# Performance work log

Measured on AMD Instinct MI355X. Metric: run time of the kernel, lower is better.

Reference implementation:

```python
import jax, jax.numpy as jnp
import numpy as np

B, C, N, D, E = 2048, 3, 1568, 16, 8  # batch, classes, input caps, out dim, in dim
T_ROUTING = 3


def squash(t, axis=-1):
    sq_norm = jnp.sum(t * t, axis=axis, keepdims=True)
    return (sq_norm / (1.0 + sq_norm)) * t / jnp.sqrt(sq_norm)


def setup_inputs() -> dict:
    key = jax.random.key(0)
    k1, k2 = jax.random.split(key)
    x = jax.random.normal(k1, (B, N, E), dtype=jnp.float32)
    W = 0.001 * jax.random.normal(k2, (1, C, N, D, E), dtype=jnp.float32)
    return {"x": x, "W": W}


def reference(x, W):
    # u_hat = W @ x[:, None, :, :, None]  -> (B, C, N, D) (trailing 1-dim dropped)
    u = jnp.einsum('ocnde,bne->bcnd', W, x)
    b = jnp.zeros((B, C, N), dtype=u.dtype)  # routing logits
    v = None
    for _ in range(T_ROUTING):
        c = jax.nn.softmax(b, axis=1)               # coupling coeffs over classes
        s = jnp.einsum('bcnd,bcn->bcd', u, c)       # weighted sum over input caps
        v = squash(s)                               # (B, C, D)
        b = b + jnp.einsum('bcd,bcnd->bcn', v, u)   # agreement update
    return v
```

## Files before the change

kernel.cpp:

```cpp
#include <hip/hip_runtime.h>
#include <hip/hip_fp16.h>

#define BB 2048
#define NN 1568
#define CD 48

__device__ __forceinline__ unsigned packh2(float a, float b) {
    __half2 h = __floats2half2_rn(a, b);
    unsigned r; __builtin_memcpy(&r, &h, 4); return r;
}
__device__ __forceinline__ float2 uph2(unsigned v) {
    __half2 h; __builtin_memcpy(&h, &v, 4); return __half22float2(h);
}

__global__ __launch_bounds__(256, 3)
void k1_u(const float* __restrict__ x, const float* __restrict__ W,
          __half* __restrict__ u)
{
    __shared__ float wlds[16 * 384];
    const int t  = threadIdx.x;
    const int bl = t & 31;
    const int h  = (t >> 5) & 1;
    const int ns = t >> 6;
    const int bg = blockIdx.x & 63;
    const int g  = blockIdx.x >> 6;
    const int b  = bg * 32 + bl;
    const int n0 = g * 16;

    float xr[32];
#pragma unroll
    for (int i = 0; i < 4; ++i) {
        const float* xp = x + ((size_t)b * NN + n0 + ns * 4 + i) * 8;
        const float4 a = __ldg((const float4*)xp);
        const float4 c = __ldg((const float4*)(xp + 4));
        xr[i*8+0]=a.x; xr[i*8+1]=a.y; xr[i*8+2]=a.z; xr[i*8+3]=a.w;
        xr[i*8+4]=c.x; xr[i*8+5]=c.y; xr[i*8+6]=c.z; xr[i*8+7]=c.w;
    }

#pragma unroll
    for (int k = 0; k < 6; ++k) {
        const int q = t + k * 256;
        const int c = q >> 9;
        const int j = (q >> 5) & 15;
        const int f = q & 31;
        const float4 v = *(const float4*)(W + (((size_t)(c * NN + n0 + j)) << 7) + (f << 2));
        *(float4*)(wlds + j * 384 + c * 128 + (f << 2)) = v;
    }
    __syncthreads();

#pragma unroll
    for (int i = 0; i < 4; ++i) {
        const int nr = ns * 4 + i;
        const int n  = n0 + nr;
        const float x0 = xr[i*8+0], x1 = xr[i*8+1], x2 = xr[i*8+2], x3 = xr[i*8+3];
        const float x4 = xr[i*8+4], x5 = xr[i*8+5], x6 = xr[i*8+6], x7 = xr[i*8+7];
        __half* dst = u + ((size_t)b * NN + n) * CD + h * 8;

#pragma unroll
        for (int c = 0; c < 3; ++c) {
            const float* wc = wlds + nr * 384 + c * 128 + h * 64;
            uint4 pk;
#pragma unroll
            for (int pp = 0; pp < 4; ++pp) {
                const float4 w0 = *(const float4*)(wc + 16 * pp);
                const float4 w1 = *(const float4*)(wc + 16 * pp + 4);
                const float4 w2 = *(const float4*)(wc + 16 * pp + 8);
                const float4 w3 = *(const float4*)(wc + 16 * pp + 12);
                const float a0 = w0.x*x0 + w0.y*x1 + w0.z*x2 + w0.w*x3
                               + w1.x*x4 + w1.y*x5 + w1.z*x6 + w1.w*x7;
                const float a1 = w2.x*x0 + w2.y*x1 + w2.z*x2 + w2.w*x3
                               + w3.x*x4 + w3.y*x5 + w3.z*x6 + w3.w*x7;
                const unsigned pv = packh2(a0, a1);
                if (pp == 0) pk.x = pv; else if (pp == 1) pk.y = pv;
                else if (pp == 2) pk.z = pv; else pk.w = pv;
            }
            *(uint4*)(dst + c * 16) = pk;
        }
    }
}

__global__ __launch_bounds__(256, 3)
void k2_route(const __half* __restrict__ u, float* __restrict__ out)
{
    __shared__ float red[4][CD];
    __shared__ float vsh[CD];

    const int t = threadIdx.x;
    const int w = t >> 6;
    const int b = blockIdx.x;
    const __half* ub = u + (size_t)b * NN * CD;

    float acc[CD];

#pragma unroll
    for (int i = 0; i < CD; ++i) acc[i] = 0.f;
    for (int n = t; n < NN; n += 256) {
        const uint4* p = (const uint4*)(ub + (size_t)n * CD);
        const uint4 r0 = p[0], r1 = p[1], r2 = p[2], r3 = p[3], r4 = p[4], r5 = p[5];
        const unsigned rr[24] = { r0.x,r0.y,r0.z,r0.w, r1.x,r1.y,r1.z,r1.w,
                                  r2.x,r2.y,r2.z,r2.w, r3.x,r3.y,r3.z,r3.w,
                                  r4.x,r4.y,r4.z,r4.w, r5.x,r5.y,r5.z,r5.w };
#pragma unroll
        for (int j = 0; j < 24; ++j) {
            const float2 f = uph2(rr[j]);
            acc[2*j] += f.x; acc[2*j+1] += f.y;
        }
    }
#pragma unroll
    for (int i = 0; i < CD; ++i) {
        float v = acc[i];
        v += __shfl_xor(v, 1); v += __shfl_xor(v, 2); v += __shfl_xor(v, 4);
        v += __shfl_xor(v, 8); v += __shfl_xor(v, 16); v += __shfl_xor(v, 32);
        acc[i] = v;
    }
    if ((t & 63) == 0) { for (int i = 0; i < CD; ++i) red[w][i] = acc[i]; }
    __syncthreads();
    if (t < CD) {
        float s = (red[0][t] + red[1][t] + red[2][t] + red[3][t]) * (1.0f / 3.0f);
        float q = s * s;
        q += __shfl_xor(q, 1); q += __shfl_xor(q, 2); q += __shfl_xor(q, 4); q += __shfl_xor(q, 8);
        vsh[t] = s * sqrtf(q) / (1.f + q);
    }
    __syncthreads();

#pragma unroll 1
    for (int pass = 1; pass <= 2; ++pass) {
        float wv[CD];
#pragma unroll
        for (int i = 0; i < CD; ++i) wv[i] = vsh[i];
#pragma unroll
        for (int i = 0; i < CD; ++i) acc[i] = 0.f;

        for (int n = t; n < NN; n += 256) {
            const uint4* p = (const uint4*)(ub + (size_t)n * CD);
            const uint4 r0 = p[0], r1 = p[1], r2 = p[2], r3 = p[3], r4 = p[4], r5 = p[5];
            const unsigned rr[24] = { r0.x,r0.y,r0.z,r0.w, r1.x,r1.y,r1.z,r1.w,
                                      r2.x,r2.y,r2.z,r2.w, r3.x,r3.y,r3.z,r3.w,
                                      r4.x,r4.y,r4.z,r4.w, r5.x,r5.y,r5.z,r5.w };
            float l0 = 0.f, l1 = 0.f, l2 = 0.f;
#pragma unroll
            for (int j = 0; j < 8; ++j) {
                const float2 f0 = uph2(rr[j]);
                const float2 f1 = uph2(rr[8 + j]);
                const float2 f2 = uph2(rr[16 + j]);
                l0 += wv[2*j]      * f0.x + wv[2*j+1]      * f0.y;
                l1 += wv[16+2*j]   * f1.x + wv[16+2*j+1]   * f1.y;
                l2 += wv[32+2*j]   * f2.x + wv[32+2*j+1]   * f2.y;
            }
            const float e0 = __expf(l0), e1 = __expf(l1), e2 = __expf(l2);
            const float inv = 1.f / (e0 + e1 + e2);
            const float c0 = e0 * inv, c1 = e1 * inv, c2 = e2 * inv;
#pragma unroll
            for (int j = 0; j < 8; ++j) {
                const float2 f0 = uph2(rr[j]);
                const float2 f1 = uph2(rr[8 + j]);
                const float2 f2 = uph2(rr[16 + j]);
                acc[2*j]      += c0 * f0.x;  acc[2*j+1]      += c0 * f0.y;
                acc[16+2*j]   += c1 * f1.x;  acc[16+2*j+1]   += c1 * f1.y;
                acc[32+2*j]   += c2 * f2.x;  acc[32+2*j+1]   += c2 * f2.y;
            }
        }
#pragma unroll
        for (int i = 0; i < CD; ++i) {
            float v = acc[i];
            v += __shfl_xor(v, 1); v += __shfl_xor(v, 2); v += __shfl_xor(v, 4);
            v += __shfl_xor(v, 8); v += __shfl_xor(v, 16); v += __shfl_xor(v, 32);
            acc[i] = v;
        }
        if ((t & 63) == 0) { for (int i = 0; i < CD; ++i) red[w][i] = acc[i]; }
        __syncthreads();
        if (t < CD) {
            const float s = red[0][t] + red[1][t] + red[2][t] + red[3][t];
            float q = s * s;
            q += __shfl_xor(q, 1); q += __shfl_xor(q, 2); q += __shfl_xor(q, 4); q += __shfl_xor(q, 8);
            const float v = s * sqrtf(q) / (1.f + q);
            if (pass == 1) vsh[t] = wv[t] + v;
            else           out[b * CD + t] = v;
        }
        __syncthreads();
    }
}

extern "C" void kernel_launch(void* const* d_in, const int* in_sizes, int n_in,
                              void* d_out, int out_size, void* d_ws, size_t ws_size,
                              hipStream_t stream) {
    (void)in_sizes; (void)n_in; (void)out_size;
    const float* x = (const float*)d_in[0];
    const float* W = (const float*)d_in[1];
    const size_t u_bytes = (size_t)BB * NN * CD * sizeof(__half);
    if (ws_size < u_bytes) return;
    __half* u = (__half*)d_ws;

    hipLaunchKernelGGL(k1_u,     dim3(98 * 64), dim3(256), 0, stream, x, W, u);
    hipLaunchKernelGGL(k2_route, dim3(BB),      dim3(256), 0, stream, u, (float*)d_out);
}
```

Baseline: 435.4 us.

## Fuse u_hat computation into routing kernel with per-batch LDS-resident u

Removes the global fp16 u_hat buffer (about 300 MB written and then read three times). A small pre-kernel converts W to fp16 in a coalesced layout. Each batch block then computes u_hat into LDS (about 157 KB) and runs all routing passes from LDS. The cost is one block per CU with 512 threads, W being re-read from L2 by every batch block, and fp16 rounding of W, which adds error.

```diff
diff --git a/kernel.cpp b/kernel.cpp
--- a/kernel.cpp
+++ b/kernel.cpp
@@ -4,6 +4,8 @@
 #define BB 2048
 #define NN 1568
 #define CD 48
+#define TPB 512
+#define WSLOTS 98304
 
 __device__ __forceinline__ unsigned packh2(float a, float b) {
     __half2 h = __floats2half2_rn(a, b);
@@ -13,110 +15,110 @@
     __half2 h; __builtin_memcpy(&h, &v, 4); return __half22float2(h);
 }
 
-__global__ __launch_bounds__(256, 3)
-void k1_u(const float* __restrict__ x, const float* __restrict__ W,
-          __half* __restrict__ u)
+__global__ __launch_bounds__(256)
+void wcast(const float* __restrict__ W, uint4* __restrict__ Wh)
 {
-    __shared__ float wlds[16 * 384];
-    const int t  = threadIdx.x;
-    const int bl = t & 31;
-    const int h  = (t >> 5) & 1;
-    const int ns = t >> 6;
-    const int bg = blockIdx.x & 63;
-    const int g  = blockIdx.x >> 6;
-    const int b  = bg * 32 + bl;
-    const int n0 = g * 16;
-
-    float xr[32];
+    const int id = blockIdx.x * 256 + threadIdx.x;
+    const int ts = id & 511;
+    const int r  = id >> 9;
+    const int dq = r & 3;
+    const int ci = r >> 2;
+    const int i  = ci & 3;
+    const int c  = ci >> 2;
+    const int n  = i * 512 + ts;
+    uint4* dst = Wh + (size_t)ci * 8192 + dq * 4 * 512 + ts;
+    if (n < NN) {
+        const float* src = W + ((size_t)(c * NN + n)) * 128 + dq * 32;
 #pragma unroll
-    for (int i = 0; i < 4; ++i) {
-        const float* xp = x + ((size_t)b * NN + n0 + ns * 4 + i) * 8;
-        const float4 a = __ldg((const float4*)xp);
-        const float4 c = __ldg((const float4*)(xp + 4));
-        xr[i*8+0]=a.x; xr[i*8+1]=a.y; xr[i*8+2]=a.z; xr[i*8+3]=a.w;
-        xr[i*8+4]=c.x; xr[i*8+5]=c.y; xr[i*8+6]=c.z; xr[i*8+7]=c.w;
-    }
-
+        for (int dd = 0; dd < 4; ++dd) {
+            const float4 f0 = *(const float4*)(src + dd * 8);
+            const float4 f1 = *(const float4*)(src + dd * 8 + 4);
+            uint4 q;
+            q.x = packh2(f0.x, f0.y); q.y = packh2(f0.z, f0.w);
+            q.z = packh2(f1.x, f1.y); q.w = packh2(f1.z, f1.w);
+            dst[dd * 512] = q;
+        }
+    } else {
+        const uint4 z = make_uint4(0u, 0u, 0u, 0u);
 #pragma unroll
-    for (int k = 0; k < 6; ++k) {
-        const int q = t + k * 256;
-        const int c = q >> 9;
-        const int j = (q >> 5) & 15;
-        const int f = q & 31;
-        const float4 v = *(const float4*)(W + (((size_t)(c * NN + n0 + j)) << 7) + (f << 2));
-        *(float4*)(wlds + j * 384 + c * 128 + (f << 2)) = v;
-    }
-    __syncthreads();
-
-#pragma unroll
-    for (int i = 0; i < 4; ++i) {
-        const int nr = ns * 4 + i;
-        const int n  = n0 + nr;
-        const float x0 = xr[i*8+0], x1 = xr[i*8+1], x2 = xr[i*8+2], x3 = xr[i*8+3];
-        const float x4 = xr[i*8+4], x5 = xr[i*8+5], x6 = xr[i*8+6], x7 = xr[i*8+7];
-        __half* dst = u + ((size_t)b * NN + n) * CD + h * 8;
-
-#pragma unroll
-        for (int c = 0; c < 3; ++c) {
-            const float* wc = wlds + nr * 384 + c * 128 + h * 64;
-            uint4 pk;
-#pragma unroll
-            for (int pp = 0; pp < 4; ++pp) {
-                const float4 w0 = *(const float4*)(wc + 16 * pp);
-                const float4 w1 = *(const float4*)(wc + 16 * pp + 4);
-                const float4 w2 = *(const float4*)(wc + 16 * pp + 8);
-                const float4 w3 = *(const float4*)(wc + 16 * pp + 12);
-                const float a0 = w0.x*x0 + w0.y*x1 + w0.z*x2 + w0.w*x3
-                               + w1.x*x4 + w1.y*x5 + w1.z*x6 + w1.w*x7;
-                const float a1 = w2.x*x0 + w2.y*x1 + w2.z*x2 + w2.w*x3
-                               + w3.x*x4 + w3.y*x5 + w3.z*x6 + w3.w*x7;
-                const unsigned pv = packh2(a0, a1);
-                if (pp == 0) pk.x = pv; else if (pp == 1) pk.y = pv;
-                else if (pp == 2) pk.z = pv; else pk.w = pv;
-            }
-            *(uint4*)(dst + c * 16) = pk;
-        }
+        for (int dd = 0; dd < 4; ++dd) dst[dd * 512] = z;
     }
 }
 
-__global__ __launch_bounds__(256, 3)
-void k2_route(const __half* __restrict__ u, float* __restrict__ out)
+__global__ __launch_bounds__(TPB, 1)
+void fused(const float* __restrict__ x, const uint4* __restrict__ Wh,
+           float* __restrict__ out)
 {
-    __shared__ float red[4][CD];
+    __shared__ unsigned ul[NN * 25];
+    __shared__ float red[8][CD];
     __shared__ float vsh[CD];
 
     const int t = threadIdx.x;
     const int w = t >> 6;
     const int b = blockIdx.x;
-    const __half* ub = u + (size_t)b * NN * CD;
+    const float* xb = x + (size_t)b * NN * 8;
 
     float acc[CD];
+#pragma unroll
+    for (int j = 0; j < CD; ++j) acc[j] = 0.f;
 
-#pragma unroll
-    for (int i = 0; i < CD; ++i) acc[i] = 0.f;
-    for (int n = t; n < NN; n += 256) {
-        const uint4* p = (const uint4*)(ub + (size_t)n * CD);
-        const uint4 r0 = p[0], r1 = p[1], r2 = p[2], r3 = p[3], r4 = p[4], r5 = p[5];
-        const unsigned rr[24] = { r0.x,r0.y,r0.z,r0.w, r1.x,r1.y,r1.z,r1.w,
-                                  r2.x,r2.y,r2.z,r2.w, r3.x,r3.y,r3.z,r3.w,
-                                  r4.x,r4.y,r4.z,r4.w, r5.x,r5.y,r5.z,r5.w };
-#pragma unroll
-        for (int j = 0; j < 24; ++j) {
-            const float2 f = uph2(rr[j]);
-            acc[2*j] += f.x; acc[2*j+1] += f.y;
+#pragma unroll 1
+    for (int i = 0; i < 4; ++i) {
+        const int n = i * 512 + t;
+        if (n < NN) {
+            const float4 xa = __ldg((const float4*)(xb + n * 8));
+            const float4 xc = __ldg((const float4*)(xb + n * 8 + 4));
+            const float x0 = xa.x, x1 = xa.y, x2 = xa.z, x3 = xa.w;
+            const float x4 = xc.x, x5 = xc.y, x6 = xc.z, x7 = xc.w;
+            unsigned* row = ul + n * 25;
+
+#define DO_C(C3) { \
+            const uint4* wp = Wh + (size_t)((C3) * 4 + i) * 8192 + t; \
+            uint4 wr[16]; \
+            _Pragma("unroll") \
+            for (int d = 0; d < 16; ++d) wr[d] = wp[d * 512]; \
+            float uv[16]; \
+            _Pragma("unroll") \
+            for (int d = 0; d < 16; ++d) { \
+                const float2 p0 = uph2(wr[d].x); \
+                const float2 p1 = uph2(wr[d].y); \
+                const float2 p2 = uph2(wr[d].z); \
+                const float2 p3 = uph2(wr[d].w); \
+                uv[d] = p0.x*x0 + p0.y*x1 + p1.x*x2 + p1.y*x3 \
+                      + p2.x*x4 + p2.y*x5 + p3.x*x6 + p3.y*x7; \
+                acc[(C3) * 16 + d] += uv[d]; \
+            } \
+            _Pragma("unroll") \
+            for (int k = 0; k < 8; ++k) \
+                row[(C3) * 8 + k] = packh2(uv[2*k], uv[2*k+1]); }
+
+            DO_C(0)
+            DO_C(1)
+            DO_C(2)
+#undef DO_C
         }
     }
-#pragma unroll
-    for (int i = 0; i < CD; ++i) {
-        float v = acc[i];
-        v += __shfl_xor(v, 1); v += __shfl_xor(v, 2); v += __shfl_xor(v, 4);
-        v += __shfl_xor(v, 8); v += __shfl_xor(v, 16); v += __shfl_xor(v, 32);
-        acc[i] = v;
-    }
-    if ((t & 63) == 0) { for (int i = 0; i < CD; ++i) red[w][i] = acc[i]; }
+    __syncthreads();
+
+#define REDUCE_ACC(ARR) { \
+    _Pragma("unroll") \
+    for (int j = 0; j < CD; ++j) { \
+        float v_ = ARR[j]; \
+        v_ += __shfl_xor(v_, 1);  v_ += __shfl_xor(v_, 2); \
+        v_ += __shfl_xor(v_, 4);  v_ += __shfl_xor(v_, 8); \
+        v_ += __shfl_xor(v_, 16); v_ += __shfl_xor(v_, 32); \
+        ARR[j] = v_; \
+    } \
+    if ((t & 63) == 0) { \
+        _Pragma("unroll") \
+        for (int j = 0; j < CD; ++j) red[w][j] = ARR[j]; \
+    } }
+
+    REDUCE_ACC(acc)
     __syncthreads();
     if (t < CD) {
-        float s = (red[0][t] + red[1][t] + red[2][t] + red[3][t]) * (1.0f / 3.0f);
+        const float s = (red[0][t] + red[1][t] + red[2][t] + red[3][t]
+                       + red[4][t] + red[5][t] + red[6][t] + red[7][t]) * (1.0f / 3.0f);
         float q = s * s;
         q += __shfl_xor(q, 1); q += __shfl_xor(q, 2); q += __shfl_xor(q, 4); q += __shfl_xor(q, 8);
         vsh[t] = s * sqrtf(q) / (1.f + q);
@@ -127,58 +129,51 @@
     for (int pass = 1; pass <= 2; ++pass) {
         float wv[CD];
 #pragma unroll
-        for (int i = 0; i < CD; ++i) wv[i] = vsh[i];
+        for (int j = 0; j < CD; ++j) wv[j] = vsh[j];
+        float ac2[CD];
 #pragma unroll
-        for (int i = 0; i < CD; ++i) acc[i] = 0.f;
+        for (int j = 0; j < CD; ++j) ac2[j] = 0.f;
 
-        for (int n = t; n < NN; n += 256) {
-            const uint4* p = (const uint4*)(ub + (size_t)n * CD);
-            const uint4 r0 = p[0], r1 = p[1], r2 = p[2], r3 = p[3], r4 = p[4], r5 = p[5];
-            const unsigned rr[24] = { r0.x,r0.y,r0.z,r0.w, r1.x,r1.y,r1.z,r1.w,
-                                      r2.x,r2.y,r2.z,r2.w, r3.x,r3.y,r3.z,r3.w,
-                                      r4.x,r4.y,r4.z,r4.w, r5.x,r5.y,r5.z,r5.w };
-            float l0 = 0.f, l1 = 0.f, l2 = 0.f;
+#pragma unroll 1
+        for (int i = 0; i < 4; ++i) {
+            const int n = i * 512 + t;
+            if (n < NN) {
+                const unsigned* row = ul + n * 25;
+                float2 f[24];
 #pragma unroll
-            for (int j = 0; j < 8; ++j) {
-                const float2 f0 = uph2(rr[j]);
-                const float2 f1 = uph2(rr[8 + j]);
-                const float2 f2 = uph2(rr[16 + j]);
-                l0 += wv[2*j]      * f0.x + wv[2*j+1]      * f0.y;
-                l1 += wv[16+2*j]   * f1.x + wv[16+2*j+1]   * f1.y;
-                l2 += wv[32+2*j]   * f2.x + wv[32+2*j+1]   * f2.y;
-            }
-            const float e0 = __expf(l0), e1 = __expf(l1), e2 = __expf(l2);
-            const float inv = 1.f / (e0 + e1 + e2);
-            const float c0 = e0 * inv, c1 = e1 * inv, c2 = e2 * inv;
+                for (int j = 0; j < 24; ++j) f[j] = uph2(row[j]);
+                float l0 = 0.f, l1 = 0.f, l2 = 0.f;
 #pragma unroll
-            for (int j = 0; j < 8; ++j) {
-                const float2 f0 = uph2(rr[j]);
-                const float2 f1 = uph2(rr[8 + j]);
-                const float2 f2 = uph2(rr[16 + j]);
-                acc[2*j]      += c0 * f0.x;  acc[2*j+1]      += c0 * f0.y;
-                acc[16+2*j]   += c1 * f1.x;  acc[16+2*j+1]   += c1 * f1.y;
-                acc[32+2*j]   += c2 * f2.x;  acc[32+2*j+1]   += c2 * f2.y;
+                for (int j = 0; j < 8; ++j) {
+                    l0 += wv[2*j]      * f[j].x      + wv[2*j+1]      * f[j].y;
+                    l1 += wv[16+2*j]   * f[8+j].x    + wv[16+2*j+1]   * f[8+j].y;
+                    l2 += wv[32+2*j]   * f[16+j].x   + wv[32+2*j+1]   * f[16+j].y;
+                }
+                const float e0 = __expf(l0), e1 = __expf(l1), e2 = __expf(l2);
+                const float inv = 1.f / (e0 + e1 + e2);
+                const float c0 = e0 * inv, c1 = e1 * inv, c2 = e2 * inv;
+#pragma unroll
+                for (int j = 0; j < 8; ++j) {
+                    ac2[2*j]      += c0 * f[j].x;      ac2[2*j+1]      += c0 * f[j].y;
+                    ac2[16+2*j]   += c1 * f[8+j].x;    ac2[16+2*j+1]   += c1 * f[8+j].y;
+                    ac2[32+2*j]   += c2 * f[16+j].x;   ac2[32+2*j+1]   += c2 * f[16+j].y;
+                }
             }
         }
-#pragma unroll
-        for (int i = 0; i < CD; ++i) {
-            float v = acc[i];
-            v += __shfl_xor(v, 1); v += __shfl_xor(v, 2); v += __shfl_xor(v, 4);
-            v += __shfl_xor(v, 8); v += __shfl_xor(v, 16); v += __shfl_xor(v, 32);
-            acc[i] = v;
-        }
-        if ((t & 63) == 0) { for (int i = 0; i < CD; ++i) red[w][i] = acc[i]; }
+        REDUCE_ACC(ac2)
         __syncthreads();
         if (t < CD) {
-            const float s = red[0][t] + red[1][t] + red[2][t] + red[3][t];
+            const float s = red[0][t] + red[1][t] + red[2][t] + red[3][t]
+                          + red[4][t] + red[5][t] + red[6][t] + red[7][t];
             float q = s * s;
             q += __shfl_xor(q, 1); q += __shfl_xor(q, 2); q += __shfl_xor(q, 4); q += __shfl_xor(q, 8);
             const float v = s * sqrtf(q) / (1.f + q);
-            if (pass == 1) vsh[t] = wv[t] + v;
-            else           out[b * CD + t] = v;
+            if (pass == 1) vsh[t] += v;
+            else           out[(size_t)b * CD + t] = v;
         }
         __syncthreads();
     }
+#undef REDUCE_ACC
 }
 
 extern "C" void kernel_launch(void* const* d_in, const int* in_sizes, int n_in,
@@ -187,10 +182,9 @@
     (void)in_sizes; (void)n_in; (void)out_size;
     const float* x = (const float*)d_in[0];
     const float* W = (const float*)d_in[1];
-    const size_t u_bytes = (size_t)BB * NN * CD * sizeof(__half);
-    if (ws_size < u_bytes) return;
-    __half* u = (__half*)d_ws;
+    if (ws_size < (size_t)WSLOTS * 16) return;
+    uint4* Wh = (uint4*)d_ws;
 
-    hipLaunchKernelGGL(k1_u,     dim3(98 * 64), dim3(256), 0, stream, x, W, u);
-    hipLaunchKernelGGL(k2_route, dim3(BB),      dim3(256), 0, stream, u, (float*)d_out);
+    hipLaunchKernelGGL(wcast, dim3(96),   dim3(256), 0, stream, W, Wh);
+    hipLaunchKernelGGL(fused, dim3(BB),   dim3(TPB), 0, stream, x, Wh, (float*)d_out);
 }
```

Result: faster. 408.5 us (-6.2%).
